# Kernel optimization log

Measured on AMD Instinct MI355X. Metric: run time of the kernel, lower is better.

Reference implementation:

```python
import jax, jax.numpy as jnp
import numpy as np

HIDDEN = 256
NUM_CLASSES = 25
INPUT_DIM = 76


def _lstm_layer(x, Wi, Wh, b):
    """Flax OptimizedLSTMCell semantics: gates [i, f, g, o], zero-init carry.
    x: [B, T, D]; Wi: [D, 4H]; Wh: [H, 4H]; b: [4H]. Returns hidden seq [B, T, H]."""
    B = x.shape[0]
    H = Wh.shape[0]
    c0 = jnp.zeros((B, H), x.dtype)
    h0 = jnp.zeros((B, H), x.dtype)

    def step(carry, xt):
        c, h = carry
        z = xt @ Wi + h @ Wh + b  # [B, 4H]
        i, f, g, o = jnp.split(z, 4, axis=-1)
        i = jax.nn.sigmoid(i)
        f = jax.nn.sigmoid(f)
        g = jnp.tanh(g)
        o = jax.nn.sigmoid(o)
        c = f * c + i * g
        h = o * jnp.tanh(c)
        return (c, h), h

    (_, _), ys = jax.lax.scan(step, (c0, h0), jnp.swapaxes(x, 0, 1))  # scan over time
    return jnp.swapaxes(ys, 0, 1)  # [B, T, H]


def setup_inputs() -> dict:
    key = jax.random.key(0)
    ks = jax.random.split(key, 9)
    B, T, D, H = 512, 512, INPUT_DIM, HIDDEN
    s_in = 1.0 / np.sqrt(D)
    s_h = 1.0 / np.sqrt(H)
    return {
        "x": jax.random.normal(ks[0], (B, T, D), jnp.float32),
        "Wi1": jax.random.normal(ks[1], (D, 4 * H), jnp.float32) * s_in,
        "Wh1": jax.random.normal(ks[2], (H, 4 * H), jnp.float32) * s_h,
        "b1": jnp.zeros((4 * H,), jnp.float32),
        "Wi2": jax.random.normal(ks[3], (H, 4 * H), jnp.float32) * s_h,
        "Wh2": jax.random.normal(ks[4], (H, 4 * H), jnp.float32) * s_h,
        "b2": jnp.zeros((4 * H,), jnp.float32),
        "Wd": jax.random.normal(ks[5], (H, NUM_CLASSES), jnp.float32) * s_h,
        "bd": jnp.zeros((NUM_CLASSES,), jnp.float32),
    }


def reference(x, Wi1, Wh1, b1, Wi2, Wh2, b2, Wd, bd):
    h1 = _lstm_layer(x, Wi1, Wh1, b1)   # [B, T, H]
    h2 = _lstm_layer(h1, Wi2, Wh2, b2)  # [B, T, H]
    feats = h2[:, -1]                   # dropout deterministic (eval mode)
    logits = feats @ Wd + bd            # [B, num_classes]
    return logits
```

## Files before the change

### kernel.cpp

```cpp
#include <hip/hip_runtime.h>

#define BB 512
#define TT 512
#define DD 76
#define HH 256
#define NC 25
#define NBLK 256
#define NTHREADS 512
#define BBHH (BB * HH)

#define K1 352
#define K2 512
#define WS1 360
#define WS2 520

typedef unsigned short u16;
typedef unsigned int u32;
typedef unsigned long long u64;
typedef __attribute__((ext_vector_type(8))) short bf16x8;
typedef __attribute__((ext_vector_type(4))) float f32x4;

__device__ __forceinline__ float bf2f(u16 v) {
  union { u32 u; float f; } c; c.u = ((u32)v) << 16; return c.f;
}
__device__ __forceinline__ u16 f2bf(float f) {
  union { u32 u; float f; } c; c.f = f;
  u32 r = c.u + 0x7FFFu + ((c.u >> 16) & 1u);
  return (u16)(r >> 16);
}
__device__ __forceinline__ void split2(float f, u16& h, u16& l) {
  u16 hh = f2bf(f);
  float r = f - bf2f(hh);
  h = hh; l = f2bf(r);
}
__device__ __forceinline__ float tanh_f(float v) {
  float e = __expf(2.0f * v);
  return 1.0f - 2.0f / (e + 1.0f);
}
__device__ __forceinline__ float gact(float v, bool is_tanh) {
  float e = __expf(is_tanh ? 2.0f * v : -v);
  float inv = 1.0f / (1.0f + e);
  return is_tanh ? 1.0f - 2.0f * inv : inv;
}

__device__ __forceinline__ u64 ald2(const u32* p) {
  return __hip_atomic_load((const u64*)p, __ATOMIC_RELAXED, __HIP_MEMORY_SCOPE_AGENT);
}
__device__ __forceinline__ u32 ald1(const u32* p) {
  return __hip_atomic_load(p, __ATOMIC_RELAXED, __HIP_MEMORY_SCOPE_AGENT);
}
__device__ __forceinline__ void ast1(u32* p, u32 v) {
  __hip_atomic_store(p, v, __ATOMIC_RELAXED, __HIP_MEMORY_SCOPE_AGENT);
}
__device__ __forceinline__ void ast2(u64* p, u64 v) {
  __hip_atomic_store(p, v, __ATOMIC_RELAXED, __HIP_MEMORY_SCOPE_AGENT);
}

__device__ __forceinline__ void wait_flags(const u32* fbase, u32 target) {
  const int tid = threadIdx.x;
  if (tid < 32) {
    const u32* p = fbase + tid * 32;
    while (__hip_atomic_load(p, __ATOMIC_RELAXED, __HIP_MEMORY_SCOPE_AGENT) < target)
      __builtin_amdgcn_s_sleep(1);
  }
  __syncthreads();
}
__device__ __forceinline__ void post_flag(u32* slot, u32 val) {
  __syncthreads();
  if (threadIdx.x == 0) ast1(slot, val);
}

__device__ __forceinline__ bf16x8 hi8(const u64 w[4]) {
  union { u32 u[4]; bf16x8 v; } c;
#pragma unroll
  for (int i = 0; i < 4; ++i)
    c.u[i] = __builtin_amdgcn_perm((u32)(w[i] >> 32), (u32)w[i], 0x05040100u);
  return c.v;
}
__device__ __forceinline__ bf16x8 lo8(const u64 w[4]) {
  union { u32 u[4]; bf16x8 v; } c;
#pragma unroll
  for (int i = 0; i < 4; ++i)
    c.u[i] = __builtin_amdgcn_perm((u32)(w[i] >> 32), (u32)w[i], 0x07060302u);
  return c.v;
}

__device__ __forceinline__ void splitv8(const float* f, bf16x8& vh, bf16x8& vl) {
  union { u16 s[8]; bf16x8 v; } ch, cl;
#pragma unroll
  for (int i = 0; i < 8; ++i) { u16 h_, l_; split2(f[i], h_, l_); ch.s[i] = h_; cl.s[i] = l_; }
  vh = ch.v; vl = cl.v;
}

__global__ void repack_kernel(const float* __restrict__ Wi1, const float* __restrict__ Wh1,
                              const float* __restrict__ Wi2, const float* __restrict__ Wh2,
                              u16* __restrict__ w1hg, u16* __restrict__ w1lg,
                              u16* __restrict__ w2hg, u16* __restrict__ w2lg) {
  int idx = blockIdx.x * blockDim.x + threadIdx.x;
  const int N1 = 1024 * K1;
  if (idx < N1) {
    int c = idx / K1, k = idx - c * K1;
    int src = (c & 3) * HH + (c >> 2);
    float v = 0.f;
    if (k < HH) v = Wh1[k * 1024 + src];
    else if (k < HH + DD) v = Wi1[(k - HH) * 1024 + src];
    u16 h, l; split2(v, h, l);
    w1hg[idx] = h; w1lg[idx] = l;
  } else if (idx < N1 + 1024 * K2) {
    int d = idx - N1;
    int c = d >> 9, k = d & 511;
    int src = (c & 3) * HH + (c >> 2);
    float v = (k < HH) ? Wi2[k * 1024 + src] : Wh2[(k - HH) * 1024 + src];
    u16 h, l; split2(v, h, l);
    w2hg[d] = h; w2lg[d] = l;
  }
}

#define MFMA3(AA, AB, AC, AH, AL, BH, BL)                                   \
  { (AA) = __builtin_amdgcn_mfma_f32_16x16x32_bf16(AH, BH, (AA), 0, 0, 0);  \
    (AB) = __builtin_amdgcn_mfma_f32_16x16x32_bf16(AH, BL, (AB), 0, 0, 0);  \
    (AC) = __builtin_amdgcn_mfma_f32_16x16x32_bf16(AL, BH, (AC), 0, 0, 0); }

#define MFMA_CH(AH, AL, PH0, PL0, PH1, PL1, KOFF)                           \
  { bf16x8 b0h_ = *(const bf16x8*)((PH0) + (KOFF));                         \
    bf16x8 b0l_ = *(const bf16x8*)((PL0) + (KOFF));                         \
    bf16x8 b1h_ = *(const bf16x8*)((PH1) + (KOFF));                         \
    bf16x8 b1l_ = *(const bf16x8*)((PL1) + (KOFF));                         \
    MFMA3(aA0, aB0, aC0, AH, AL, b0h_, b0l_)                                \
    MFMA3(aA1, aB1, aC1, AH, AL, b1h_, b1l_) }

#define GATES_ST(Z, CS, DST)                                                \
  { u32 hwv[4];                                                             \
    _Pragma("unroll")                                                       \
    for (int r = 0; r < 4; ++r) {                                           \
      float a_ = gact((Z)[r], gi == 2);                                     \
      float v1_ = __shfl_xor(a_, 1);                                        \
      float v2_ = __shfl_xor(a_, 2);                                        \
      float v3_ = __shfl_xor(a_, 3);                                        \
      float cn_ = v1_ * (CS)[r] + a_ * v2_;                                 \
      (CS)[r] = cn_;                                                        \
      float hv_ = v3_ * tanh_f(cn_);                                        \
      u16 hh_, hl_; split2(hv_, hh_, hl_);                                  \
      hwv[r] = (u32)hh_ | ((u32)hl_ << 16);                                 \
    }                                                                       \
    _Pragma("unroll")                                                       \
    for (int r = 0; r < 4; ++r) {                                           \
      int base_ = lane & 48;                                                \
      u32 w1_ = __shfl(hwv[r], base_ + 4);                                  \
      u32 w2_ = __shfl(hwv[r], base_ + 8);                                  \
      u32 w3_ = __shfl(hwv[r], base_ + 12);                                 \
      if (nl == 0) {                                                        \
        u64* dp_ = (u64*)((DST) + (size_t)(rbase + r) * HH + jt * 8 + kh * 4); \
        ast2(dp_,     (u64)hwv[r] | ((u64)w1_ << 32));                      \
        ast2(dp_ + 1, (u64)w2_    | ((u64)w3_ << 32));                      \
      }                                                                     \
    }                                                                       \
  }

#define LOAD_RW(RW, BASEPTR)                                                \
  { const u32* hp_ = (BASEPTR) + (size_t)arow * HH + kh * 128;              \
    _Pragma("unroll")                                                       \
    for (int i_ = 0; i_ < 4; ++i_) {                                        \
      const u32* p_ = hp_ + i_ * 32 + qd * 8;                               \
      (RW)[i_][0] = ald2(p_);     (RW)[i_][1] = ald2(p_ + 2);               \
      (RW)[i_][2] = ald2(p_ + 4); (RW)[i_][3] = ald2(p_ + 6);               \
    } }

__global__ __launch_bounds__(NTHREADS, 2) void lstm_kernel(
    const float* __restrict__ x,
    const float* __restrict__ b1, const float* __restrict__ b2,
    const float* __restrict__ Wd, const float* __restrict__ bd,
    const u16* __restrict__ w1hg, const u16* __restrict__ w1lg,
    const u16* __restrict__ w2hg, const u16* __restrict__ w2lg,
    u32* __restrict__ h1w, u32* __restrict__ h2w,
    u32* __restrict__ flags,
    float* __restrict__ out)
{
  __shared__ u16 w1h[32 * WS1], w1l[32 * WS1];
  __shared__ u16 w2h[32 * WS2], w2l[32 * WS2];
  __shared__ float zx[2][8][64][4];

  const int tid = threadIdx.x;
  const int lane = tid & 63;
  const int wv = tid >> 6;
  const int m  = wv & 3;
  const int kh = wv >> 2;
  const int nl = lane & 15;
  const int qd = lane >> 4;
  const int bt = blockIdx.x & 7;
  const int jt = blockIdx.x >> 3;
  const int row0 = bt * 64;

  u32* gAp = flags + bt * 1024;
  u32* gBp = flags + 8192 + bt * 1024;
  u32* gAslot = gAp + jt * 32;
  u32* gBslot = gBp + jt * 32;

  for (int i = tid; i < 32 * (K1 / 2); i += NTHREADS) {
    int c = i / 176, kk = i - c * 176;
    ((u32*)&w1h[c * WS1])[kk] = ((const u32*)(w1hg + (size_t)(jt * 32 + c) * K1))[kk];
    ((u32*)&w1l[c * WS1])[kk] = ((const u32*)(w1lg + (size_t)(jt * 32 + c) * K1))[kk];
  }
  for (int i = tid; i < 32 * (K2 / 2); i += NTHREADS) {
    int c = i >> 8, kk = i & 255;
    ((u32*)&w2h[c * WS2])[kk] = ((const u32*)(w2hg + (size_t)(jt * 32 + c) * K2))[kk];
    ((u32*)&w2l[c * WS2])[kk] = ((const u32*)(w2lg + (size_t)(jt * 32 + c) * K2))[kk];
  }

  const int cg_col = jt * 32 + kh * 16 + nl;
  const int gi = cg_col & 3;
  const int rbase = row0 + m * 16 + qd * 4;

  float ab1[2], ab2[2];
#pragma unroll
  for (int tl = 0; tl < 2; ++tl) {
    int col = jt * 32 + tl * 16 + nl;
    float v1 = b1[(col & 3) * HH + (col >> 2)];
    float v2 = b2[(col & 3) * HH + (col >> 2)];
    ab1[tl] = (kh == 0) ? v1 : 0.f;
    ab2[tl] = (kh == 0) ? v2 : 0.f;
  }

  const int arow = row0 + m * 16 + nl;

  const u16* pB1h0 = w1h + nl * WS1;
  const u16* pB1l0 = w1l + nl * WS1;
  const u16* pB1h1 = w1h + (16 + nl) * WS1;
  const u16* pB1l1 = w1l + (16 + nl) * WS1;
  const u16* pB2h0 = w2h + nl * WS2;
  const u16* pB2l0 = w2l + nl * WS2;
  const u16* pB2h1 = w2h + (16 + nl) * WS2;
  const u16* pB2l1 = w2l + (16 + nl) * WS2;

  float cs1[4] = {0.f, 0.f, 0.f, 0.f}, cs2[4] = {0.f, 0.f, 0.f, 0.f};
  u64 rwh1[4][4];
  bf16x8 h1fh[4], h1fl[4];

  __syncthreads();

  {
    f32x4 aA0 = {ab1[0], ab1[0], ab1[0], ab1[0]};
    f32x4 aA1 = {ab1[1], ab1[1], ab1[1], ab1[1]};
    f32x4 aB0 = {0,0,0,0}, aB1 = {0,0,0,0}, aC0 = {0,0,0,0}, aC1 = {0,0,0,0};
    const float* xrow = x + (size_t)arow * TT * DD;
    if (kh == 0) {
#pragma unroll
      for (int ci = 0; ci < 2; ++ci) {
        float xv[8];
        float4 f0 = *(const float4*)(xrow + ci * 32 + qd * 8);
        float4 f1 = *(const float4*)(xrow + ci * 32 + qd * 8 + 4);
        xv[0]=f0.x; xv[1]=f0.y; xv[2]=f0.z; xv[3]=f0.w;
        xv[4]=f1.x; xv[5]=f1.y; xv[6]=f1.z; xv[7]=f1.w;
        bf16x8 xh, xl; splitv8(xv, xh, xl);
        const int koff = (8 + ci) * 32 + qd * 8;
        MFMA_CH(xh, xl, pB1h0, pB1l0, pB1h1, pB1l1, koff)
      }
    } else {
      float xv[8] = {0,0,0,0,0,0,0,0};
      if (qd == 0) {
        float4 f0 = *(const float4*)(xrow + 64);
        float4 f1 = *(const float4*)(xrow + 68);
        xv[0]=f0.x; xv[1]=f0.y; xv[2]=f0.z; xv[3]=f0.w;
        xv[4]=f1.x; xv[5]=f1.y; xv[6]=f1.z; xv[7]=f1.w;
      } else if (qd == 1) {
        float4 f0 = *(const float4*)(xrow + 72);
        xv[0]=f0.x; xv[1]=f0.y; xv[2]=f0.z; xv[3]=f0.w;
      }
      bf16x8 xh, xl; splitv8(xv, xh, xl);
      const int koff = 10 * 32 + qd * 8;
      MFMA_CH(xh, xl, pB1h0, pB1l0, pB1h1, pB1l1, koff)
    }
    f32x4 zk = (kh == 0) ? (aA0 + aB0 + aC0) : (aA1 + aB1 + aC1);
    f32x4 zo = (kh == 0) ? (aA1 + aB1 + aC1) : (aA0 + aB0 + aC0);
    *(f32x4*)&zx[1][wv][lane][0] = zo;
    __syncthreads();
    zk += *(const f32x4*)&zx[1][wv ^ 4][lane][0];
    GATES_ST(zk, cs1, h1w)
    __syncthreads();
    if (tid == 0) { ast1(gAslot, 1u); ast1(gBslot, 1u); }
    wait_flags(gBp, 1);
    LOAD_RW(rwh1, h1w)
  }

#pragma unroll 1
  for (int t = 0; t < TT; ++t) {
    u32* h1nw = h1w + ((t + 1) & 1) * BBHH;
    const u32* h2pw = h2w + ((t + 1) & 1) * BBHH;
    u32* h2cw = h2w + (t & 1) * BBHH;

#pragma unroll
    for (int i = 0; i < 4; ++i) { h1fh[i] = hi8(rwh1[i]); h1fl[i] = lo8(rwh1[i]); }

    if (t < TT - 1) {
      f32x4 aA0 = {ab1[0], ab1[0], ab1[0], ab1[0]};
      f32x4 aA1 = {ab1[1], ab1[1], ab1[1], ab1[1]};
      f32x4 aB0 = {0,0,0,0}, aB1 = {0,0,0,0}, aC0 = {0,0,0,0}, aC1 = {0,0,0,0};
      const float* xrow = x + ((size_t)arow * TT + (t + 1)) * DD;

      float4 xf0, xf1, xf2, xf3;
      if (kh == 0) {
        xf0 = *(const float4*)(xrow + qd * 8);
        xf1 = *(const float4*)(xrow + qd * 8 + 4);
        xf2 = *(const float4*)(xrow + 32 + qd * 8);
        xf3 = *(const float4*)(xrow + 32 + qd * 8 + 4);
      } else {
        xf0 = make_float4(0,0,0,0); xf1 = make_float4(0,0,0,0);
        if (qd == 0) {
          xf0 = *(const float4*)(xrow + 64);
          xf1 = *(const float4*)(xrow + 68);
        } else if (qd == 1) {
          xf0 = *(const float4*)(xrow + 72);
        }
      }

#pragma unroll
      for (int i = 0; i < 4; ++i) {
        const int koff = (kh * 4 + i) * 32 + qd * 8;
        MFMA_CH(h1fh[i], h1fl[i], pB1h0, pB1l0, pB1h1, pB1l1, koff)
      }
      if (kh == 0) {
        float xv[8];
        xv[0]=xf0.x; xv[1]=xf0.y; xv[2]=xf0.z; xv[3]=xf0.w;
        xv[4]=xf1.x; xv[5]=xf1.y; xv[6]=xf1.z; xv[7]=xf1.w;
        bf16x8 xh, xl; splitv8(xv, xh, xl);
        MFMA_CH(xh, xl, pB1h0, pB1l0, pB1h1, pB1l1, 8 * 32 + qd * 8)
        xv[0]=xf2.x; xv[1]=xf2.y; xv[2]=xf2.z; xv[3]=xf2.w;
        xv[4]=xf3.x; xv[5]=xf3.y; xv[6]=xf3.z; xv[7]=xf3.w;
        splitv8(xv, xh, xl);
        MFMA_CH(xh, xl, pB1h0, pB1l0, pB1h1, pB1l1, 9 * 32 + qd * 8)
      } else {
        float xv[8];
        xv[0]=xf0.x; xv[1]=xf0.y; xv[2]=xf0.z; xv[3]=xf0.w;
        xv[4]=xf1.x; xv[5]=xf1.y; xv[6]=xf1.z; xv[7]=xf1.w;
        bf16x8 xh, xl; splitv8(xv, xh, xl);
        MFMA_CH(xh, xl, pB1h0, pB1l0, pB1h1, pB1l1, 10 * 32 + qd * 8)
      }
      f32x4 zk = (kh == 0) ? (aA0 + aB0 + aC0) : (aA1 + aB1 + aC1);
      f32x4 zo = (kh == 0) ? (aA1 + aB1 + aC1) : (aA0 + aB0 + aC0);
      *(f32x4*)&zx[1][wv][lane][0] = zo;
      __syncthreads();
      zk += *(const f32x4*)&zx[1][wv ^ 4][lane][0];
      GATES_ST(zk, cs1, h1nw)
      post_flag(gBslot, t + 2);
    }

    {
      f32x4 aA0 = {ab2[0], ab2[0], ab2[0], ab2[0]};
      f32x4 aA1 = {ab2[1], ab2[1], ab2[1], ab2[1]};
      f32x4 aB0 = {0,0,0,0}, aB1 = {0,0,0,0}, aC0 = {0,0,0,0}, aC1 = {0,0,0,0};

      wait_flags(gAp, t + 1);
      if (t > 0) {
        u64 rw2[4][4];
        LOAD_RW(rw2, h2pw)
#pragma unroll
        for (int i = 0; i < 4; ++i) {
          bf16x8 ah = hi8(rw2[i]), al = lo8(rw2[i]);
          const int koff = (8 + kh * 4 + i) * 32 + qd * 8;
          MFMA_CH(ah, al, pB2h0, pB2l0, pB2h1, pB2l1, koff)
        }
      }
#pragma unroll
      for (int i = 0; i < 4; ++i) {
        const int koff = (kh * 4 + i) * 32 + qd * 8;
        MFMA_CH(h1fh[i], h1fl[i], pB2h0, pB2l0, pB2h1, pB2l1, koff)
      }
      if (t < TT - 1) {
        wait_flags(gBp, t + 2);
        LOAD_RW(rwh1, h1nw)
      }
      f32x4 zk = (kh == 0) ? (aA0 + aB0 + aC0) : (aA1 + aB1 + aC1);
      f32x4 zo = (kh == 0) ? (aA1 + aB1 + aC1) : (aA0 + aB0 + aC0);
      *(f32x4*)&zx[0][wv][lane][0] = zo;
      __syncthreads();
      zk += *(const f32x4*)&zx[0][wv ^ 4][lane][0];
      GATES_ST(zk, cs2, h2cw)
      post_flag(gAslot, t + 2);
    }
  }

  wait_flags(gAp, TT + 1);
  if (tid < 2 * NC) {
    int r = row0 + jt * 2 + tid / NC;
    int n = tid - (tid / NC) * NC;
    float s = bd[n];
    const u32* fw = h2w + BBHH + (size_t)r * HH;
#pragma unroll 8
    for (int k = 0; k < HH; ++k) {
      u32 w = ald1(fw + k);
      s += (bf2f((u16)w) + bf2f((u16)(w >> 16))) * Wd[k * NC + n];
    }
    out[r * NC + n] = s;
  }
}

extern "C" void kernel_launch(void* const* d_in, const int* in_sizes, int n_in,
                              void* d_out, int out_size, void* d_ws, size_t ws_size,
                              hipStream_t stream) {
  const float* x   = (const float*)d_in[0];
  const float* Wi1 = (const float*)d_in[1];
  const float* Wh1 = (const float*)d_in[2];
  const float* b1  = (const float*)d_in[3];
  const float* Wi2 = (const float*)d_in[4];
  const float* Wh2 = (const float*)d_in[5];
  const float* b2  = (const float*)d_in[6];
  const float* Wd  = (const float*)d_in[7];
  const float* bd  = (const float*)d_in[8];

  char* ws = (char*)d_ws;
  u32* h1w = (u32*)(ws);
  u32* h2w = (u32*)(ws + 1048576u);
  u16* w1hg = (u16*)(ws + 2097152u);
  u16* w1lg = (u16*)(ws + 2097152u + 720896u);
  u16* w2hg = (u16*)(ws + 2097152u + 2u * 720896u);
  u16* w2lg = (u16*)(ws + 2097152u + 2u * 720896u + 1048576u);
  u32* flags = (u32*)(ws + 5636096u);
  float* out = (float*)d_out;

  hipMemsetAsync((void*)flags, 0, 65536, stream);
  const int total = 1024 * K1 + 1024 * K2;
  repack_kernel<<<(total + 255) / 256, 256, 0, stream>>>(
      Wi1, Wh1, Wi2, Wh2, w1hg, w1lg, w2hg, w2lg);

  void* args[] = {
    (void*)&x, (void*)&b1, (void*)&b2, (void*)&Wd, (void*)&bd,
    (void*)&w1hg, (void*)&w1lg, (void*)&w2hg, (void*)&w2lg,
    (void*)&h1w, (void*)&h2w,
    (void*)&flags, (void*)&out
  };
  (void)hipLaunchCooperativeKernel((void*)lstm_kernel, dim3(NBLK),
                                   dim3(NTHREADS), args, 0, stream);
}
```

Before: 5.653 ms.

## Split layer-1 and layer-2 LSTM into concurrent warp groups with per-wave flags

Instead of having all eight waves of a block compute layer 1 and then layer 2 in lockstep with a K-split reduced through shared memory, waves 0-3 now run the layer-1 recurrence and waves 4-7 run layer-2, each over the full K. The two layers are pipelined through a 4-deep h1 ring buffer. Block-wide __syncthreads and LDS reductions are replaced by per-wave, per-row-group flags that are spin-waited and posted at wave level. The aim is to overlap the two layers' serial chains and cut block-level barrier cost. In exchange, each wave does twice the MFMA work per step, uses more registers (launch bounds drop the 2-blocks hint), and needs more flag and workspace memory.

```diff
diff --git a/kernel.cpp b/kernel.cpp
--- a/kernel.cpp
+++ b/kernel.cpp
@@ -6,7 +6,7 @@
 #define HH 256
 #define NC 25
 #define NBLK 256
-#define NTHREADS 512
+#define NTH 512
 #define BBHH (BB * HH)
 
 #define K1 352
@@ -56,18 +56,17 @@
   __hip_atomic_store(p, v, __ATOMIC_RELAXED, __HIP_MEMORY_SCOPE_AGENT);
 }
 
-__device__ __forceinline__ void wait_flags(const u32* fbase, u32 target) {
-  const int tid = threadIdx.x;
-  if (tid < 32) {
-    const u32* p = fbase + tid * 32;
+__device__ __forceinline__ void wwait32(const u32* base, u32 target) {
+  if ((threadIdx.x & 63) < 32) {
+    const u32* p = base + (threadIdx.x & 63) * 16;
     while (__hip_atomic_load(p, __ATOMIC_RELAXED, __HIP_MEMORY_SCOPE_AGENT) < target)
       __builtin_amdgcn_s_sleep(1);
   }
-  __syncthreads();
-}
-__device__ __forceinline__ void post_flag(u32* slot, u32 val) {
-  __syncthreads();
-  if (threadIdx.x == 0) ast1(slot, val);
+  asm volatile("" ::: "memory");
+}
+__device__ __forceinline__ void wpost(u32* slot, u32 val) {
+  asm volatile("s_waitcnt vmcnt(0)" ::: "memory");
+  if ((threadIdx.x & 63) == 0) ast1(slot, val);
 }
 
 __device__ __forceinline__ bf16x8 hi8(const u64 w[4]) {
@@ -116,57 +115,88 @@
   }
 }
 
-#define MFMA3(AA, AB, AC, AH, AL, BH, BL)                                   \
-  { (AA) = __builtin_amdgcn_mfma_f32_16x16x32_bf16(AH, BH, (AA), 0, 0, 0);  \
-    (AB) = __builtin_amdgcn_mfma_f32_16x16x32_bf16(AH, BL, (AB), 0, 0, 0);  \
-    (AC) = __builtin_amdgcn_mfma_f32_16x16x32_bf16(AL, BH, (AC), 0, 0, 0); }
-
-#define MFMA_CH(AH, AL, PH0, PL0, PH1, PL1, KOFF)                           \
-  { bf16x8 b0h_ = *(const bf16x8*)((PH0) + (KOFF));                         \
-    bf16x8 b0l_ = *(const bf16x8*)((PL0) + (KOFF));                         \
-    bf16x8 b1h_ = *(const bf16x8*)((PH1) + (KOFF));                         \
-    bf16x8 b1l_ = *(const bf16x8*)((PL1) + (KOFF));                         \
-    MFMA3(aA0, aB0, aC0, AH, AL, b0h_, b0l_)                                \
-    MFMA3(aA1, aB1, aC1, AH, AL, b1h_, b1l_) }
-
-#define GATES_ST(Z, CS, DST)                                                \
-  { u32 hwv[4];                                                             \
+#define MCH2(AH, AL, KOFF)                                                  \
+  { bf16x8 b0h_ = *(const bf16x8*)(p0h + (KOFF));                           \
+    bf16x8 b0l_ = *(const bf16x8*)(p0l + (KOFF));                           \
+    bf16x8 b1h_ = *(const bf16x8*)(p1h + (KOFF));                           \
+    bf16x8 b1l_ = *(const bf16x8*)(p1l + (KOFF));                           \
+    a0A = __builtin_amdgcn_mfma_f32_16x16x32_bf16(AH, b0h_, a0A, 0, 0, 0);  \
+    a0B = __builtin_amdgcn_mfma_f32_16x16x32_bf16(AH, b0l_, a0B, 0, 0, 0);  \
+    a0C = __builtin_amdgcn_mfma_f32_16x16x32_bf16(AL, b0h_, a0C, 0, 0, 0);  \
+    a1A = __builtin_amdgcn_mfma_f32_16x16x32_bf16(AH, b1h_, a1A, 0, 0, 0);  \
+    a1B = __builtin_amdgcn_mfma_f32_16x16x32_bf16(AH, b1l_, a1B, 0, 0, 0);  \
+    a1C = __builtin_amdgcn_mfma_f32_16x16x32_bf16(AL, b1h_, a1C, 0, 0, 0); }
+
+#define GATES2T(Z0, Z1, CS0, CS1, DST)                                      \
+  { u32 g0v[4], g1v[4];                                                     \
     _Pragma("unroll")                                                       \
     for (int r = 0; r < 4; ++r) {                                           \
-      float a_ = gact((Z)[r], gi == 2);                                     \
-      float v1_ = __shfl_xor(a_, 1);                                        \
-      float v2_ = __shfl_xor(a_, 2);                                        \
-      float v3_ = __shfl_xor(a_, 3);                                        \
-      float cn_ = v1_ * (CS)[r] + a_ * v2_;                                 \
-      (CS)[r] = cn_;                                                        \
-      float hv_ = v3_ * tanh_f(cn_);                                        \
-      u16 hh_, hl_; split2(hv_, hh_, hl_);                                  \
-      hwv[r] = (u32)hh_ | ((u32)hl_ << 16);                                 \
+      float a0_ = gact((Z0)[r], gi == 2);                                   \
+      float p01 = __shfl_xor(a0_, 1), p02 = __shfl_xor(a0_, 2), p03 = __shfl_xor(a0_, 3); \
+      float c0_ = p01 * (CS0)[r] + a0_ * p02;                               \
+      (CS0)[r] = c0_;                                                       \
+      float h0_ = p03 * tanh_f(c0_);                                        \
+      u16 hh0_, hl0_; split2(h0_, hh0_, hl0_);                              \
+      g0v[r] = (u32)hh0_ | ((u32)hl0_ << 16);                               \
+      float a1_ = gact((Z1)[r], gi == 2);                                   \
+      float p11 = __shfl_xor(a1_, 1), p12 = __shfl_xor(a1_, 2), p13 = __shfl_xor(a1_, 3); \
+      float c1_ = p11 * (CS1)[r] + a1_ * p12;                               \
+      (CS1)[r] = c1_;                                                       \
+      float h1_ = p13 * tanh_f(c1_);                                        \
+      u16 hh1_, hl1_; split2(h1_, hh1_, hl1_);                              \
+      g1v[r] = (u32)hh1_ | ((u32)hl1_ << 16);                               \
     }                                                                       \
     _Pragma("unroll")                                                       \
     for (int r = 0; r < 4; ++r) {                                           \
       int base_ = lane & 48;                                                \
-      u32 w1_ = __shfl(hwv[r], base_ + 4);                                  \
-      u32 w2_ = __shfl(hwv[r], base_ + 8);                                  \
-      u32 w3_ = __shfl(hwv[r], base_ + 12);                                 \
+      u32 a1_ = __shfl(g0v[r], base_ + 4);                                  \
+      u32 a2_ = __shfl(g0v[r], base_ + 8);                                  \
+      u32 a3_ = __shfl(g0v[r], base_ + 12);                                 \
+      u32 b1_ = __shfl(g1v[r], base_ + 4);                                  \
+      u32 b2_ = __shfl(g1v[r], base_ + 8);                                  \
+      u32 b3_ = __shfl(g1v[r], base_ + 12);                                 \
       if (nl == 0) {                                                        \
-        u64* dp_ = (u64*)((DST) + (size_t)(rbase + r) * HH + jt * 8 + kh * 4); \
-        ast2(dp_,     (u64)hwv[r] | ((u64)w1_ << 32));                      \
-        ast2(dp_ + 1, (u64)w2_    | ((u64)w3_ << 32));                      \
+        u64* dp_ = (u64*)((DST) + (size_t)(rbase + r) * HH + jt * 8);       \
+        ast2(dp_,     (u64)g0v[r] | ((u64)a1_ << 32));                      \
+        ast2(dp_ + 1, (u64)a2_    | ((u64)a3_ << 32));                      \
+        ast2(dp_ + 2, (u64)g1v[r] | ((u64)b1_ << 32));                      \
+        ast2(dp_ + 3, (u64)b2_    | ((u64)b3_ << 32));                      \
       }                                                                     \
     }                                                                       \
   }
 
-#define LOAD_RW(RW, BASEPTR)                                                \
-  { const u32* hp_ = (BASEPTR) + (size_t)arow * HH + kh * 128;              \
+#define LOAD_RW8(RW, BASEPTR)                                               \
+  { const u32* hp_ = (BASEPTR) + (size_t)arow * HH;                         \
     _Pragma("unroll")                                                       \
-    for (int i_ = 0; i_ < 4; ++i_) {                                        \
+    for (int i_ = 0; i_ < 8; ++i_) {                                        \
       const u32* p_ = hp_ + i_ * 32 + qd * 8;                               \
       (RW)[i_][0] = ald2(p_);     (RW)[i_][1] = ald2(p_ + 2);               \
       (RW)[i_][2] = ald2(p_ + 4); (RW)[i_][3] = ald2(p_ + 6);               \
     } }
 
-__global__ __launch_bounds__(NTHREADS, 2) void lstm_kernel(
+#define X_LOAD(XROW)                                                        \
+    float4 xa0 = *(const float4*)((XROW) + qd * 8);                         \
+    float4 xa1 = *(const float4*)((XROW) + qd * 8 + 4);                     \
+    float4 xb0 = *(const float4*)((XROW) + 32 + qd * 8);                    \
+    float4 xb1 = *(const float4*)((XROW) + 32 + qd * 8 + 4);                \
+    float4 xc0 = make_float4(0,0,0,0), xc1 = make_float4(0,0,0,0);          \
+    if (qd == 0) { xc0 = *(const float4*)((XROW) + 64);                     \
+                   xc1 = *(const float4*)((XROW) + 68); }                   \
+    else if (qd == 1) { xc0 = *(const float4*)((XROW) + 72); }
+
+#define X_MFMA2()                                                           \
+  { float xv[8]; bf16x8 xh, xl;                                             \
+    xv[0]=xa0.x; xv[1]=xa0.y; xv[2]=xa0.z; xv[3]=xa0.w;                     \
+    xv[4]=xa1.x; xv[5]=xa1.y; xv[6]=xa1.z; xv[7]=xa1.w;                     \
+    splitv8(xv, xh, xl); MCH2(xh, xl, 8 * 32 + qd * 8)                      \
+    xv[0]=xb0.x; xv[1]=xb0.y; xv[2]=xb0.z; xv[3]=xb0.w;                     \
+    xv[4]=xb1.x; xv[5]=xb1.y; xv[6]=xb1.z; xv[7]=xb1.w;                     \
+    splitv8(xv, xh, xl); MCH2(xh, xl, 9 * 32 + qd * 8)                      \
+    xv[0]=xc0.x; xv[1]=xc0.y; xv[2]=xc0.z; xv[3]=xc0.w;                     \
+    xv[4]=xc1.x; xv[5]=xc1.y; xv[6]=xc1.z; xv[7]=xc1.w;                     \
+    splitv8(xv, xh, xl); MCH2(xh, xl, 10 * 32 + qd * 8) }
+
+__global__ __launch_bounds__(NTH) void lstm_kernel(
     const float* __restrict__ x,
     const float* __restrict__ b1, const float* __restrict__ b2,
     const float* __restrict__ Wd, const float* __restrict__ bd,
@@ -178,219 +208,127 @@
 {
   __shared__ u16 w1h[32 * WS1], w1l[32 * WS1];
   __shared__ u16 w2h[32 * WS2], w2l[32 * WS2];
-  __shared__ float zx[2][8][64][4];
 
   const int tid = threadIdx.x;
   const int lane = tid & 63;
   const int wv = tid >> 6;
   const int m  = wv & 3;
-  const int kh = wv >> 2;
+  const int grp = wv >> 2;
   const int nl = lane & 15;
   const int qd = lane >> 4;
   const int bt = blockIdx.x & 7;
   const int jt = blockIdx.x >> 3;
   const int row0 = bt * 64;
 
-  u32* gAp = flags + bt * 1024;
-  u32* gBp = flags + 8192 + bt * 1024;
-  u32* gAslot = gAp + jt * 32;
-  u32* gBslot = gBp + jt * 32;
-
-  for (int i = tid; i < 32 * (K1 / 2); i += NTHREADS) {
+  for (int i = tid; i < 32 * (K1 / 2); i += NTH) {
     int c = i / 176, kk = i - c * 176;
     ((u32*)&w1h[c * WS1])[kk] = ((const u32*)(w1hg + (size_t)(jt * 32 + c) * K1))[kk];
     ((u32*)&w1l[c * WS1])[kk] = ((const u32*)(w1lg + (size_t)(jt * 32 + c) * K1))[kk];
   }
-  for (int i = tid; i < 32 * (K2 / 2); i += NTHREADS) {
+  for (int i = tid; i < 32 * (K2 / 2); i += NTH) {
     int c = i >> 8, kk = i & 255;
     ((u32*)&w2h[c * WS2])[kk] = ((const u32*)(w2hg + (size_t)(jt * 32 + c) * K2))[kk];
     ((u32*)&w2l[c * WS2])[kk] = ((const u32*)(w2lg + (size_t)(jt * 32 + c) * K2))[kk];
   }
-
-  const int cg_col = jt * 32 + kh * 16 + nl;
-  const int gi = cg_col & 3;
+  __syncthreads();
+
+  const int gi = nl & 3;
   const int rbase = row0 + m * 16 + qd * 4;
-
-  float ab1[2], ab2[2];
-#pragma unroll
-  for (int tl = 0; tl < 2; ++tl) {
-    int col = jt * 32 + tl * 16 + nl;
-    float v1 = b1[(col & 3) * HH + (col >> 2)];
-    float v2 = b2[(col & 3) * HH + (col >> 2)];
-    ab1[tl] = (kh == 0) ? v1 : 0.f;
-    ab2[tl] = (kh == 0) ? v2 : 0.f;
-  }
-
   const int arow = row0 + m * 16 + nl;
 
-  const u16* pB1h0 = w1h + nl * WS1;
-  const u16* pB1l0 = w1l + nl * WS1;
-  const u16* pB1h1 = w1h + (16 + nl) * WS1;
-  const u16* pB1l1 = w1l + (16 + nl) * WS1;
-  const u16* pB2h0 = w2h + nl * WS2;
-  const u16* pB2l0 = w2l + nl * WS2;
-  const u16* pB2h1 = w2h + (16 + nl) * WS2;
-  const u16* pB2l1 = w2l + (16 + nl) * WS2;
-
-  float cs1[4] = {0.f, 0.f, 0.f, 0.f}, cs2[4] = {0.f, 0.f, 0.f, 0.f};
-  u64 rwh1[4][4];
-  bf16x8 h1fh[4], h1fl[4];
-
-  __syncthreads();
-
-  {
-    f32x4 aA0 = {ab1[0], ab1[0], ab1[0], ab1[0]};
-    f32x4 aA1 = {ab1[1], ab1[1], ab1[1], ab1[1]};
-    f32x4 aB0 = {0,0,0,0}, aB1 = {0,0,0,0}, aC0 = {0,0,0,0}, aC1 = {0,0,0,0};
-    const float* xrow = x + (size_t)arow * TT * DD;
-    if (kh == 0) {
-#pragma unroll
-      for (int ci = 0; ci < 2; ++ci) {
-        float xv[8];
-        float4 f0 = *(const float4*)(xrow + ci * 32 + qd * 8);
-        float4 f1 = *(const float4*)(xrow + ci * 32 + qd * 8 + 4);
-        xv[0]=f0.x; xv[1]=f0.y; xv[2]=f0.z; xv[3]=f0.w;
-        xv[4]=f1.x; xv[5]=f1.y; xv[6]=f1.z; xv[7]=f1.w;
-        bf16x8 xh, xl; splitv8(xv, xh, xl);
-        const int koff = (8 + ci) * 32 + qd * 8;
-        MFMA_CH(xh, xl, pB1h0, pB1l0, pB1h1, pB1l1, koff)
-      }
-    } else {
-      float xv[8] = {0,0,0,0,0,0,0,0};
-      if (qd == 0) {
-        float4 f0 = *(const float4*)(xrow + 64);
-        float4 f1 = *(const float4*)(xrow + 68);
-        xv[0]=f0.x; xv[1]=f0.y; xv[2]=f0.z; xv[3]=f0.w;
-        xv[4]=f1.x; xv[5]=f1.y; xv[6]=f1.z; xv[7]=f1.w;
-      } else if (qd == 1) {
-        float4 f0 = *(const float4*)(xrow + 72);
-        xv[0]=f0.x; xv[1]=f0.y; xv[2]=f0.z; xv[3]=f0.w;
-      }
-      bf16x8 xh, xl; splitv8(xv, xh, xl);
-      const int koff = 10 * 32 + qd * 8;
-      MFMA_CH(xh, xl, pB1h0, pB1l0, pB1h1, pB1l1, koff)
+  u32* fA = flags;
+  u32* fB = flags + 16384;
+  u32* fAm = fA + (bt * 4 + m) * 512;
+  u32* fBm = fB + (bt * 4 + m) * 512;
+  u32* fAslot = fAm + jt * 16;
+  u32* fBslot = fBm + jt * 16;
+
+  if (grp == 0) {
+    const u16* p0h = w1h + nl * WS1;
+    const u16* p0l = w1l + nl * WS1;
+    const u16* p1h = w1h + (16 + nl) * WS1;
+    const u16* p1l = w1l + (16 + nl) * WS1;
+    const float ab0 = b1[gi * HH + ((jt * 32 + nl) >> 2)];
+    const float ab1v = b1[gi * HH + ((jt * 32 + 16 + nl) >> 2)];
+    float cs0[4] = {0.f, 0.f, 0.f, 0.f}, cs1[4] = {0.f, 0.f, 0.f, 0.f};
+    u64 rw[8][4];
+
+#pragma unroll 1
+    for (int i = 0; i < TT; ++i) {
+      const float* xrow = x + ((size_t)arow * TT + i) * DD;
+      X_LOAD(xrow)
+      if (i > 0) {
+        wwait32(fBm, (u32)i);
+        LOAD_RW8(rw, h1w + (size_t)((i - 1) & 3) * BBHH)
+      }
+      if (i >= 4) wwait32(fAm, (u32)(i - 3));
+      f32x4 a0A = {ab0, ab0, ab0, ab0}, a1A = {ab1v, ab1v, ab1v, ab1v};
+      f32x4 a0B = {0,0,0,0}, a0C = {0,0,0,0}, a1B = {0,0,0,0}, a1C = {0,0,0,0};
+      if (i > 0) {
+#pragma unroll
+        for (int c = 0; c < 8; ++c) {
+          bf16x8 ah = hi8(rw[c]), al = lo8(rw[c]);
+          MCH2(ah, al, c * 32 + qd * 8)
+        }
+      }
+      X_MFMA2()
+      f32x4 z0 = a0A + a0B + a0C, z1 = a1A + a1B + a1C;
+      GATES2T(z0, z1, cs0, cs1, h1w + (size_t)(i & 3) * BBHH)
+      wpost(fBslot, (u32)(i + 1));
     }
-    f32x4 zk = (kh == 0) ? (aA0 + aB0 + aC0) : (aA1 + aB1 + aC1);
-    f32x4 zo = (kh == 0) ? (aA1 + aB1 + aC1) : (aA0 + aB0 + aC0);
-    *(f32x4*)&zx[1][wv][lane][0] = zo;
-    __syncthreads();
-    zk += *(const f32x4*)&zx[1][wv ^ 4][lane][0];
-    GATES_ST(zk, cs1, h1w)
-    __syncthreads();
-    if (tid == 0) { ast1(gAslot, 1u); ast1(gBslot, 1u); }
-    wait_flags(gBp, 1);
-    LOAD_RW(rwh1, h1w)
-  }
+  } else {
+    const u16* p0h = w2h + nl * WS2;
+    const u16* p0l = w2l + nl * WS2;
+    const u16* p1h = w2h + (16 + nl) * WS2;
+    const u16* p1l = w2l + (16 + nl) * WS2;
+    const float ab0 = b2[gi * HH + ((jt * 32 + nl) >> 2)];
+    const float ab1v = b2[gi * HH + ((jt * 32 + 16 + nl) >> 2)];
+    float cs0[4] = {0.f, 0.f, 0.f, 0.f}, cs1[4] = {0.f, 0.f, 0.f, 0.f};
+    u64 rh1[8][4], rh2[8][4];
 
 #pragma unroll 1
-  for (int t = 0; t < TT; ++t) {
-    u32* h1nw = h1w + ((t + 1) & 1) * BBHH;
-    const u32* h2pw = h2w + ((t + 1) & 1) * BBHH;
-    u32* h2cw = h2w + (t & 1) * BBHH;
-
-#pragma unroll
-    for (int i = 0; i < 4; ++i) { h1fh[i] = hi8(rwh1[i]); h1fl[i] = lo8(rwh1[i]); }
-
-    if (t < TT - 1) {
-      f32x4 aA0 = {ab1[0], ab1[0], ab1[0], ab1[0]};
-      f32x4 aA1 = {ab1[1], ab1[1], ab1[1], ab1[1]};
-      f32x4 aB0 = {0,0,0,0}, aB1 = {0,0,0,0}, aC0 = {0,0,0,0}, aC1 = {0,0,0,0};
-      const float* xrow = x + ((size_t)arow * TT + (t + 1)) * DD;
-
-      float4 xf0, xf1, xf2, xf3;
-      if (kh == 0) {
-        xf0 = *(const float4*)(xrow + qd * 8);
-        xf1 = *(const float4*)(xrow + qd * 8 + 4);
-        xf2 = *(const float4*)(xrow + 32 + qd * 8);
-        xf3 = *(const float4*)(xrow + 32 + qd * 8 + 4);
-      } else {
-        xf0 = make_float4(0,0,0,0); xf1 = make_float4(0,0,0,0);
-        if (qd == 0) {
-          xf0 = *(const float4*)(xrow + 64);
-          xf1 = *(const float4*)(xrow + 68);
-        } else if (qd == 1) {
-          xf0 = *(const float4*)(xrow + 72);
+    for (int t = 0; t < TT; ++t) {
+      wwait32(fBm, (u32)(t + 1));
+      LOAD_RW8(rh1, h1w + (size_t)(t & 3) * BBHH)
+      if (t > 0) {
+        wwait32(fAm, (u32)t);
+        LOAD_RW8(rh2, h2w + (size_t)((t - 1) & 1) * BBHH)
+      }
+      f32x4 a0A = {ab0, ab0, ab0, ab0}, a1A = {ab1v, ab1v, ab1v, ab1v};
+      f32x4 a0B = {0,0,0,0}, a0C = {0,0,0,0}, a1B = {0,0,0,0}, a1C = {0,0,0,0};
+#pragma unroll
+      for (int c = 0; c < 8; ++c) {
+        bf16x8 ah = hi8(rh1[c]), al = lo8(rh1[c]);
+        MCH2(ah, al, c * 32 + qd * 8)
+      }
+      if (t > 0) {
+#pragma unroll
+        for (int c = 0; c < 8; ++c) {
+          bf16x8 ah = hi8(rh2[c]), al = lo8(rh2[c]);
+          MCH2(ah, al, (8 + c) * 32 + qd * 8)
         }
       }
-
-#pragma unroll
-      for (int i = 0; i < 4; ++i) {
-        const int koff = (kh * 4 + i) * 32 + qd * 8;
-        MFMA_CH(h1fh[i], h1fl[i], pB1h0, pB1l0, pB1h1, pB1l1, koff)
-      }
-      if (kh == 0) {
-        float xv[8];
-        xv[0]=xf0.x; xv[1]=xf0.y; xv[2]=xf0.z; xv[3]=xf0.w;
-        xv[4]=xf1.x; xv[5]=xf1.y; xv[6]=xf1.z; xv[7]=xf1.w;
-        bf16x8 xh, xl; splitv8(xv, xh, xl);
-        MFMA_CH(xh, xl, pB1h0, pB1l0, pB1h1, pB1l1, 8 * 32 + qd * 8)
-        xv[0]=xf2.x; xv[1]=xf2.y; xv[2]=xf2.z; xv[3]=xf2.w;
-        xv[4]=xf3.x; xv[5]=xf3.y; xv[6]=xf3.z; xv[7]=xf3.w;
-        splitv8(xv, xh, xl);
-        MFMA_CH(xh, xl, pB1h0, pB1l0, pB1h1, pB1l1, 9 * 32 + qd * 8)
-      } else {
-        float xv[8];
-        xv[0]=xf0.x; xv[1]=xf0.y; xv[2]=xf0.z; xv[3]=xf0.w;
-        xv[4]=xf1.x; xv[5]=xf1.y; xv[6]=xf1.z; xv[7]=xf1.w;
-        bf16x8 xh, xl; splitv8(xv, xh, xl);
-        MFMA_CH(xh, xl, pB1h0, pB1l0, pB1h1, pB1l1, 10 * 32 + qd * 8)
-      }
-      f32x4 zk = (kh == 0) ? (aA0 + aB0 + aC0) : (aA1 + aB1 + aC1);
-      f32x4 zo = (kh == 0) ? (aA1 + aB1 + aC1) : (aA0 + aB0 + aC0);
-      *(f32x4*)&zx[1][wv][lane][0] = zo;
-      __syncthreads();
-      zk += *(const f32x4*)&zx[1][wv ^ 4][lane][0];
-      GATES_ST(zk, cs1, h1nw)
-      post_flag(gBslot, t + 2);
+      f32x4 z0 = a0A + a0B + a0C, z1 = a1A + a1B + a1C;
+      GATES2T(z0, z1, cs0, cs1, h2w + (size_t)(t & 1) * BBHH)
+      wpost(fAslot, (u32)(t + 1));
     }
 
-    {
-      f32x4 aA0 = {ab2[0], ab2[0], ab2[0], ab2[0]};
-      f32x4 aA1 = {ab2[1], ab2[1], ab2[1], ab2[1]};
-      f32x4 aB0 = {0,0,0,0}, aB1 = {0,0,0,0}, aC0 = {0,0,0,0}, aC1 = {0,0,0,0};
-
-      wait_flags(gAp, t + 1);
-      if (t > 0) {
-        u64 rw2[4][4];
-        LOAD_RW(rw2, h2pw)
-#pragma unroll
-        for (int i = 0; i < 4; ++i) {
-          bf16x8 ah = hi8(rw2[i]), al = lo8(rw2[i]);
-          const int koff = (8 + kh * 4 + i) * 32 + qd * 8;
-          MFMA_CH(ah, al, pB2h0, pB2l0, pB2h1, pB2l1, koff)
+    if (wv == 4) {
+      const int mh = jt >> 3;
+      wwait32(fA + (bt * 4 + mh) * 512, (u32)TT);
+      if (lane < 2 * NC) {
+        int r = row0 + jt * 2 + lane / NC;
+        int n = lane - (lane / NC) * NC;
+        float s = bd[n];
+        const u32* fw = h2w + BBHH + (size_t)r * HH;
+#pragma unroll 8
+        for (int k = 0; k < HH; ++k) {
+          u32 w = ald1(fw + k);
+          s += (bf2f((u16)w) + bf2f((u16)(w >> 16))) * Wd[k * NC + n];
         }
-      }
-#pragma unroll
-      for (int i = 0; i < 4; ++i) {
-        const int koff = (kh * 4 + i) * 32 + qd * 8;
-        MFMA_CH(h1fh[i], h1fl[i], pB2h0, pB2l0, pB2h1, pB2l1, koff)
-      }
-      if (t < TT - 1) {
-        wait_flags(gBp, t + 2);
-        LOAD_RW(rwh1, h1nw)
-      }
-      f32x4 zk = (kh == 0) ? (aA0 + aB0 + aC0) : (aA1 + aB1 + aC1);
-      f32x4 zo = (kh == 0) ? (aA1 + aB1 + aC1) : (aA0 + aB0 + aC0);
-      *(f32x4*)&zx[0][wv][lane][0] = zo;
-      __syncthreads();
-      zk += *(const f32x4*)&zx[0][wv ^ 4][lane][0];
-      GATES_ST(zk, cs2, h2cw)
-      post_flag(gAslot, t + 2);
+        out[r * NC + n] = s;
+      }
     }
-  }
-
-  wait_flags(gAp, TT + 1);
-  if (tid < 2 * NC) {
-    int r = row0 + jt * 2 + tid / NC;
-    int n = tid - (tid / NC) * NC;
-    float s = bd[n];
-    const u32* fw = h2w + BBHH + (size_t)r * HH;
-#pragma unroll 8
-    for (int k = 0; k < HH; ++k) {
-      u32 w = ald1(fw + k);
-      s += (bf2f((u16)w) + bf2f((u16)(w >> 16))) * Wd[k * NC + n];
-    }
-    out[r * NC + n] = s;
   }
 }
 
@@ -409,15 +347,15 @@
 
   char* ws = (char*)d_ws;
   u32* h1w = (u32*)(ws);
-  u32* h2w = (u32*)(ws + 1048576u);
-  u16* w1hg = (u16*)(ws + 2097152u);
-  u16* w1lg = (u16*)(ws + 2097152u + 720896u);
-  u16* w2hg = (u16*)(ws + 2097152u + 2u * 720896u);
-  u16* w2lg = (u16*)(ws + 2097152u + 2u * 720896u + 1048576u);
-  u32* flags = (u32*)(ws + 5636096u);
+  u32* h2w = (u32*)(ws + 2097152u);
+  u16* w1hg = (u16*)(ws + 3145728u);
+  u16* w1lg = (u16*)(ws + 3145728u + 720896u);
+  u16* w2hg = (u16*)(ws + 3145728u + 2u * 720896u);
+  u16* w2lg = (u16*)(ws + 3145728u + 2u * 720896u + 1048576u);
+  u32* flags = (u32*)(ws + 6684672u);
   float* out = (float*)d_out;
 
-  hipMemsetAsync((void*)flags, 0, 65536, stream);
+  hipMemsetAsync((void*)flags, 0, 131072, stream);
   const int total = 1024 * K1 + 1024 * K2;
   repack_kernel<<<(total + 255) / 256, 256, 0, stream>>>(
       Wi1, Wh1, Wi2, Wh2, w1hg, w1lg, w2hg, w2lg);
@@ -429,5 +367,5 @@
     (void*)&flags, (void*)&out
   };
   (void)hipLaunchCooperativeKernel((void*)lstm_kernel, dim3(NBLK),
-                                   dim3(NTHREADS), args, 0, stream);
-}
+                                   dim3(NTH), args, 0, stream);
+}
```

Result: slower. 8.715 ms (+54.2%).

## Merge layer-1 and layer-2 steps into one phase with a single flag barrier

Applied to the files above, without the earlier changes.

Restructures the time loop so each iteration computes layer-1 step t+1 and layer-2 step t together after one wait on a shared flag array. Before, each step posted and waited on two separate inter-block flags. Both hidden-state reads now happen together and a single post_flag follows both gate updates, which halves the cross-block synchronization round trips per timestep. In exchange there are more live accumulators and registers (min-blocks hint removed from launch_bounds), so occupancy or spilling could suffer.

```diff
diff --git a/kernel.cpp b/kernel.cpp
--- a/kernel.cpp
+++ b/kernel.cpp
@@ -57,9 +57,8 @@
 }
 
 __device__ __forceinline__ void wait_flags(const u32* fbase, u32 target) {
-  const int tid = threadIdx.x;
-  if (tid < 32) {
-    const u32* p = fbase + tid * 32;
+  if (threadIdx.x < 32) {
+    const u32* p = fbase + threadIdx.x * 32;
     while (__hip_atomic_load(p, __ATOMIC_RELAXED, __HIP_MEMORY_SCOPE_AGENT) < target)
       __builtin_amdgcn_s_sleep(1);
   }
@@ -116,18 +115,17 @@
   }
 }
 
-#define MFMA3(AA, AB, AC, AH, AL, BH, BL)                                   \
-  { (AA) = __builtin_amdgcn_mfma_f32_16x16x32_bf16(AH, BH, (AA), 0, 0, 0);  \
-    (AB) = __builtin_amdgcn_mfma_f32_16x16x32_bf16(AH, BL, (AB), 0, 0, 0);  \
-    (AC) = __builtin_amdgcn_mfma_f32_16x16x32_bf16(AL, BH, (AC), 0, 0, 0); }
-
-#define MFMA_CH(AH, AL, PH0, PL0, PH1, PL1, KOFF)                           \
+#define MFMA_CH6(AH, AL, PH0, PL0, PH1, PL1, KOFF, A0, B0, C0, A1, B1, C1)  \
   { bf16x8 b0h_ = *(const bf16x8*)((PH0) + (KOFF));                         \
     bf16x8 b0l_ = *(const bf16x8*)((PL0) + (KOFF));                         \
     bf16x8 b1h_ = *(const bf16x8*)((PH1) + (KOFF));                         \
     bf16x8 b1l_ = *(const bf16x8*)((PL1) + (KOFF));                         \
-    MFMA3(aA0, aB0, aC0, AH, AL, b0h_, b0l_)                                \
-    MFMA3(aA1, aB1, aC1, AH, AL, b1h_, b1l_) }
+    A0 = __builtin_amdgcn_mfma_f32_16x16x32_bf16(AH, b0h_, A0, 0, 0, 0);    \
+    B0 = __builtin_amdgcn_mfma_f32_16x16x32_bf16(AH, b0l_, B0, 0, 0, 0);    \
+    C0 = __builtin_amdgcn_mfma_f32_16x16x32_bf16(AL, b0h_, C0, 0, 0, 0);    \
+    A1 = __builtin_amdgcn_mfma_f32_16x16x32_bf16(AH, b1h_, A1, 0, 0, 0);    \
+    B1 = __builtin_amdgcn_mfma_f32_16x16x32_bf16(AH, b1l_, B1, 0, 0, 0);    \
+    C1 = __builtin_amdgcn_mfma_f32_16x16x32_bf16(AL, b1h_, C1, 0, 0, 0); }
 
 #define GATES_ST(Z, CS, DST)                                                \
   { u32 hwv[4];                                                             \
@@ -166,7 +164,7 @@
       (RW)[i_][2] = ald2(p_ + 4); (RW)[i_][3] = ald2(p_ + 6);               \
     } }
 
-__global__ __launch_bounds__(NTHREADS, 2) void lstm_kernel(
+__global__ __launch_bounds__(NTHREADS) void lstm_kernel(
     const float* __restrict__ x,
     const float* __restrict__ b1, const float* __restrict__ b2,
     const float* __restrict__ Wd, const float* __restrict__ bd,
@@ -191,10 +189,8 @@
   const int jt = blockIdx.x >> 3;
   const int row0 = bt * 64;
 
-  u32* gAp = flags + bt * 1024;
-  u32* gBp = flags + 8192 + bt * 1024;
-  u32* gAslot = gAp + jt * 32;
-  u32* gBslot = gBp + jt * 32;
+  u32* fCp = flags + bt * 1024;
+  u32* fCslot = fCp + jt * 32;
 
   for (int i = tid; i < 32 * (K1 / 2); i += NTHREADS) {
     int c = i / 176, kk = i - c * 176;
@@ -210,6 +206,7 @@
   const int cg_col = jt * 32 + kh * 16 + nl;
   const int gi = cg_col & 3;
   const int rbase = row0 + m * 16 + qd * 4;
+  const int arow = row0 + m * 16 + nl;
 
   float ab1[2], ab2[2];
 #pragma unroll
@@ -220,8 +217,6 @@
     ab1[tl] = (kh == 0) ? v1 : 0.f;
     ab2[tl] = (kh == 0) ? v2 : 0.f;
   }
-
-  const int arow = row0 + m * 16 + nl;
 
   const u16* pB1h0 = w1h + nl * WS1;
   const u16* pB1l0 = w1l + nl * WS1;
@@ -233,8 +228,7 @@
   const u16* pB2l1 = w2l + (16 + nl) * WS2;
 
   float cs1[4] = {0.f, 0.f, 0.f, 0.f}, cs2[4] = {0.f, 0.f, 0.f, 0.f};
-  u64 rwh1[4][4];
-  bf16x8 h1fh[4], h1fl[4];
+  u64 rwh1[4][4], rw2[4][4];
 
   __syncthreads();
 
@@ -253,7 +247,7 @@
         xv[4]=f1.x; xv[5]=f1.y; xv[6]=f1.z; xv[7]=f1.w;
         bf16x8 xh, xl; splitv8(xv, xh, xl);
         const int koff = (8 + ci) * 32 + qd * 8;
-        MFMA_CH(xh, xl, pB1h0, pB1l0, pB1h1, pB1l1, koff)
+        MFMA_CH6(xh, xl, pB1h0, pB1l0, pB1h1, pB1l1, koff, aA0, aB0, aC0, aA1, aB1, aC1)
       }
     } else {
       float xv[8] = {0,0,0,0,0,0,0,0};
@@ -268,7 +262,7 @@
       }
       bf16x8 xh, xl; splitv8(xv, xh, xl);
       const int koff = 10 * 32 + qd * 8;
-      MFMA_CH(xh, xl, pB1h0, pB1l0, pB1h1, pB1l1, koff)
+      MFMA_CH6(xh, xl, pB1h0, pB1l0, pB1h1, pB1l1, koff, aA0, aB0, aC0, aA1, aB1, aC1)
     }
     f32x4 zk = (kh == 0) ? (aA0 + aB0 + aC0) : (aA1 + aB1 + aC1);
     f32x4 zo = (kh == 0) ? (aA1 + aB1 + aC1) : (aA0 + aB0 + aC0);
@@ -276,28 +270,27 @@
     __syncthreads();
     zk += *(const f32x4*)&zx[1][wv ^ 4][lane][0];
     GATES_ST(zk, cs1, h1w)
-    __syncthreads();
-    if (tid == 0) { ast1(gAslot, 1u); ast1(gBslot, 1u); }
-    wait_flags(gBp, 1);
-    LOAD_RW(rwh1, h1w)
+    post_flag(fCslot, 1u);
   }
 
 #pragma unroll 1
   for (int t = 0; t < TT; ++t) {
+    const u32* h1cw = h1w + (t & 1) * BBHH;
     u32* h1nw = h1w + ((t + 1) & 1) * BBHH;
     const u32* h2pw = h2w + ((t + 1) & 1) * BBHH;
     u32* h2cw = h2w + (t & 1) * BBHH;
-
-#pragma unroll
-    for (int i = 0; i < 4; ++i) { h1fh[i] = hi8(rwh1[i]); h1fl[i] = lo8(rwh1[i]); }
-
-    if (t < TT - 1) {
-      f32x4 aA0 = {ab1[0], ab1[0], ab1[0], ab1[0]};
-      f32x4 aA1 = {ab1[1], ab1[1], ab1[1], ab1[1]};
-      f32x4 aB0 = {0,0,0,0}, aB1 = {0,0,0,0}, aC0 = {0,0,0,0}, aC1 = {0,0,0,0};
+    const bool doA = (t < TT - 1);
+
+    f32x4 aA0 = {ab1[0], ab1[0], ab1[0], ab1[0]};
+    f32x4 aA1 = {ab1[1], ab1[1], ab1[1], ab1[1]};
+    f32x4 aB0 = {0,0,0,0}, aB1 = {0,0,0,0}, aC0 = {0,0,0,0}, aC1 = {0,0,0,0};
+    f32x4 bA0 = {ab2[0], ab2[0], ab2[0], ab2[0]};
+    f32x4 bA1 = {ab2[1], ab2[1], ab2[1], ab2[1]};
+    f32x4 bB0 = {0,0,0,0}, bB1 = {0,0,0,0}, bC0 = {0,0,0,0}, bC1 = {0,0,0,0};
+
+    float4 xf0, xf1, xf2, xf3;
+    if (doA) {
       const float* xrow = x + ((size_t)arow * TT + (t + 1)) * DD;
-
-      float4 xf0, xf1, xf2, xf3;
       if (kh == 0) {
         xf0 = *(const float4*)(xrow + qd * 8);
         xf1 = *(const float4*)(xrow + qd * 8 + 4);
@@ -312,74 +305,72 @@
           xf0 = *(const float4*)(xrow + 72);
         }
       }
-
-#pragma unroll
-      for (int i = 0; i < 4; ++i) {
-        const int koff = (kh * 4 + i) * 32 + qd * 8;
-        MFMA_CH(h1fh[i], h1fl[i], pB1h0, pB1l0, pB1h1, pB1l1, koff)
-      }
+    }
+
+    wait_flags(fCp, (u32)(t + 1));
+
+    LOAD_RW(rwh1, h1cw)
+    if (t > 0) LOAD_RW(rw2, h2pw)
+
+    if (doA) {
+      float xv[8]; bf16x8 xh, xl;
       if (kh == 0) {
-        float xv[8];
         xv[0]=xf0.x; xv[1]=xf0.y; xv[2]=xf0.z; xv[3]=xf0.w;
         xv[4]=xf1.x; xv[5]=xf1.y; xv[6]=xf1.z; xv[7]=xf1.w;
-        bf16x8 xh, xl; splitv8(xv, xh, xl);
-        MFMA_CH(xh, xl, pB1h0, pB1l0, pB1h1, pB1l1, 8 * 32 + qd * 8)
+        splitv8(xv, xh, xl);
+        MFMA_CH6(xh, xl, pB1h0, pB1l0, pB1h1, pB1l1, 8 * 32 + qd * 8,
+                 aA0, aB0, aC0, aA1, aB1, aC1)
         xv[0]=xf2.x; xv[1]=xf2.y; xv[2]=xf2.z; xv[3]=xf2.w;
         xv[4]=xf3.x; xv[5]=xf3.y; xv[6]=xf3.z; xv[7]=xf3.w;
         splitv8(xv, xh, xl);
-        MFMA_CH(xh, xl, pB1h0, pB1l0, pB1h1, pB1l1, 9 * 32 + qd * 8)
+        MFMA_CH6(xh, xl, pB1h0, pB1l0, pB1h1, pB1l1, 9 * 32 + qd * 8,
+                 aA0, aB0, aC0, aA1, aB1, aC1)
       } else {
-        float xv[8];
         xv[0]=xf0.x; xv[1]=xf0.y; xv[2]=xf0.z; xv[3]=xf0.w;
         xv[4]=xf1.x; xv[5]=xf1.y; xv[6]=xf1.z; xv[7]=xf1.w;
-        bf16x8 xh, xl; splitv8(xv, xh, xl);
-        MFMA_CH(xh, xl, pB1h0, pB1l0, pB1h1, pB1l1, 10 * 32 + qd * 8)
+        splitv8(xv, xh, xl);
+        MFMA_CH6(xh, xl, pB1h0, pB1l0, pB1h1, pB1l1, 10 * 32 + qd * 8,
+                 aA0, aB0, aC0, aA1, aB1, aC1)
       }
-      f32x4 zk = (kh == 0) ? (aA0 + aB0 + aC0) : (aA1 + aB1 + aC1);
-      f32x4 zo = (kh == 0) ? (aA1 + aB1 + aC1) : (aA0 + aB0 + aC0);
-      *(f32x4*)&zx[1][wv][lane][0] = zo;
-      __syncthreads();
-      zk += *(const f32x4*)&zx[1][wv ^ 4][lane][0];
-      GATES_ST(zk, cs1, h1nw)
-      post_flag(gBslot, t + 2);
-    }
-
-    {
-      f32x4 aA0 = {ab2[0], ab2[0], ab2[0], ab2[0]};
-      f32x4 aA1 = {ab2[1], ab2[1], ab2[1], ab2[1]};
-      f32x4 aB0 = {0,0,0,0}, aB1 = {0,0,0,0}, aC0 = {0,0,0,0}, aC1 = {0,0,0,0};
-
-      wait_flags(gAp, t + 1);
-      if (t > 0) {
-        u64 rw2[4][4];
-        LOAD_RW(rw2, h2pw)
-#pragma unroll
-        for (int i = 0; i < 4; ++i) {
-          bf16x8 ah = hi8(rw2[i]), al = lo8(rw2[i]);
-          const int koff = (8 + kh * 4 + i) * 32 + qd * 8;
-          MFMA_CH(ah, al, pB2h0, pB2l0, pB2h1, pB2l1, koff)
-        }
+    }
+
+#pragma unroll
+    for (int i = 0; i < 4; ++i) {
+      bf16x8 fh = hi8(rwh1[i]), fl = lo8(rwh1[i]);
+      const int koff = (kh * 4 + i) * 32 + qd * 8;
+      if (doA)
+        MFMA_CH6(fh, fl, pB1h0, pB1l0, pB1h1, pB1l1, koff, aA0, aB0, aC0, aA1, aB1, aC1)
+      MFMA_CH6(fh, fl, pB2h0, pB2l0, pB2h1, pB2l1, koff, bA0, bB0, bC0, bA1, bB1, bC1)
+    }
+    if (t > 0) {
+#pragma unroll
+      for (int i = 0; i < 4; ++i) {
+        bf16x8 fh = hi8(rw2[i]), fl = lo8(rw2[i]);
+        const int koff = (8 + kh * 4 + i) * 32 + qd * 8;
+        MFMA_CH6(fh, fl, pB2h0, pB2l0, pB2h1, pB2l1, koff, bA0, bB0, bC0, bA1, bB1, bC1)
       }
-#pragma unroll
-      for (int i = 0; i < 4; ++i) {
-        const int koff = (kh * 4 + i) * 32 + qd * 8;
-        MFMA_CH(h1fh[i], h1fl[i], pB2h0, pB2l0, pB2h1, pB2l1, koff)
-      }
-      if (t < TT - 1) {
-        wait_flags(gBp, t + 2);
-        LOAD_RW(rwh1, h1nw)
-      }
-      f32x4 zk = (kh == 0) ? (aA0 + aB0 + aC0) : (aA1 + aB1 + aC1);
-      f32x4 zo = (kh == 0) ? (aA1 + aB1 + aC1) : (aA0 + aB0 + aC0);
-      *(f32x4*)&zx[0][wv][lane][0] = zo;
-      __syncthreads();
-      zk += *(const f32x4*)&zx[0][wv ^ 4][lane][0];
-      GATES_ST(zk, cs2, h2cw)
-      post_flag(gAslot, t + 2);
-    }
-  }
-
-  wait_flags(gAp, TT + 1);
+    }
+
+    f32x4 z2k = (kh == 0) ? (bA0 + bB0 + bC0) : (bA1 + bB1 + bC1);
+    f32x4 z2o = (kh == 0) ? (bA1 + bB1 + bC1) : (bA0 + bB0 + bC0);
+    *(f32x4*)&zx[0][wv][lane][0] = z2o;
+    f32x4 z1k = {0,0,0,0};
+    if (doA) {
+      z1k = (kh == 0) ? (aA0 + aB0 + aC0) : (aA1 + aB1 + aC1);
+      f32x4 z1o = (kh == 0) ? (aA1 + aB1 + aC1) : (aA0 + aB0 + aC0);
+      *(f32x4*)&zx[1][wv][lane][0] = z1o;
+    }
+    __syncthreads();
+    z2k += *(const f32x4*)&zx[0][wv ^ 4][lane][0];
+    if (doA) {
+      z1k += *(const f32x4*)&zx[1][wv ^ 4][lane][0];
+      GATES_ST(z1k, cs1, h1nw)
+    }
+    GATES_ST(z2k, cs2, h2cw)
+    post_flag(fCslot, (u32)(t + 2));
+  }
+
+  wait_flags(fCp, TT + 1);
   if (tid < 2 * NC) {
     int r = row0 + jt * 2 + tid / NC;
     int n = tid - (tid / NC) * NC;
```

Measured after the change: 5.481 ms. -3.1%, faster.
